# Kernel optimization log

Measured on AMD Instinct MI355X. Metric: run time of the kernel, lower is better.

## Reference

```python
import jax, jax.numpy as jnp
import numpy as np

M, IN, OUT = 8192, 4096, 4096
XOR_MASK = (1 << 3) | (1 << 7)  # 0x88: flips sign bit of each packed nibble


def _dequant_int4(weight_packed, weight_scales):
    """Decode packed int4 weights (offset-binary nibbles) to scaled float.

    weight_packed: [OUT, IN//2] int32, each byte holds two nibbles (v+8).
    Low nibble -> even input column, high nibble -> odd input column.
    """
    w = jnp.bitwise_xor(weight_packed, XOR_MASK)  # offset-binary -> two's complement nibbles
    low = jnp.bitwise_and(w, 0xF)
    high = jnp.bitwise_and(jnp.right_shift(w, 4), 0xF)
    low = jnp.where(low >= 8, low - 16, low)    # signed int4 in [-8, 7]
    high = jnp.where(high >= 8, high - 16, high)
    # interleave nibbles: [OUT, IN//2, 2] -> [OUT, IN]
    deq = jnp.stack([low, high], axis=-1).reshape(weight_packed.shape[0], -1)
    return deq.astype(weight_scales.dtype) * weight_scales[:, None]  # [OUT, IN]


def setup_inputs() -> dict:
    key = jax.random.key(0)
    k1, k2, k3, k4 = jax.random.split(key, 4)
    x = jax.random.normal(k1, (M, IN), dtype=jnp.float32)
    weight_packed = jax.random.randint(k2, (OUT, IN // 2), 0, 256, dtype=jnp.int32)
    weight_scales = jax.random.uniform(k3, (OUT,), dtype=jnp.float32) * 0.02 + 1e-3
    bias = jax.random.normal(k4, (OUT,), dtype=jnp.float32)
    return {"x": x, "weight_packed": weight_packed,
            "weight_scales": weight_scales, "bias": bias}


def reference(x, weight_packed, weight_scales, bias):
    # w4a16 forward: dequantize int4 weights per output row, then GEMM + bias.
    w = _dequant_int4(weight_packed, weight_scales)  # [OUT, IN]
    return jnp.dot(x, w.T) + bias  # [M, OUT]
```

## Files before the change

kernel.cpp:

```cpp
#include <hip/hip_runtime.h>
#include <cstdint>
#include <cstddef>

#define M_DIM 8192
#define K_DIM 4096
#define N_DIM 4096

#define BM 256
#define BN 256
#define BK 64
#define NT (K_DIM / BK)

typedef unsigned short u16;
typedef __bf16 bf16x8 __attribute__((ext_vector_type(8)));
typedef u16 u16x8 __attribute__((ext_vector_type(8)));
typedef float f32x4 __attribute__((ext_vector_type(4)));

__device__ __forceinline__ u16 f2bf_rne(float f) {
  uint32_t u = __builtin_bit_cast(uint32_t, f);
  return (u16)((u + 0x7FFFu + ((u >> 16) & 1u)) >> 16);
}
__device__ __forceinline__ u16 i2bf(int i) {
  return (u16)(__builtin_bit_cast(uint32_t, (float)i) >> 16);
}

#define XBLKS 16384
#define WBLKS 8192

__global__ __launch_bounds__(256) void prep(const float* __restrict__ x,
                                            const int* __restrict__ wp,
                                            u16* __restrict__ xb,
                                            u16* __restrict__ wb) {
  const int b = blockIdx.x;
  if (b < XBLKS) {
    size_t t = (size_t)b * 256 + threadIdx.x;
    const float4* xp = (const float4*)x;
    float4 a = xp[2 * t];
    float4 c = xp[2 * t + 1];
    u16x8 r;
    r[0] = f2bf_rne(a.x); r[1] = f2bf_rne(a.y); r[2] = f2bf_rne(a.z); r[3] = f2bf_rne(a.w);
    r[4] = f2bf_rne(c.x); r[5] = f2bf_rne(c.y); r[6] = f2bf_rne(c.z); r[7] = f2bf_rne(c.w);
    ((u16x8*)xb)[t] = r;
  } else {
    size_t t = (size_t)(b - XBLKS) * 256 + threadIdx.x;
    int4 p = ((const int4*)wp)[t];
    u16x8 r;
    int v;
    v = p.x ^ 0x88; r[0] = i2bf((v << 28) >> 28); r[1] = i2bf((v << 24) >> 28);
    v = p.y ^ 0x88; r[2] = i2bf((v << 28) >> 28); r[3] = i2bf((v << 24) >> 28);
    v = p.z ^ 0x88; r[4] = i2bf((v << 28) >> 28); r[5] = i2bf((v << 24) >> 28);
    v = p.w ^ 0x88; r[6] = i2bf((v << 28) >> 28); r[7] = i2bf((v << 24) >> 28);
    ((u16x8*)wb)[t] = r;
  }
}

__global__ __launch_bounds__(512, 2) void gemm_bt_w4a16(
    const u16* __restrict__ A,
    const u16* __restrict__ B,
    const float* __restrict__ scales,
    const float* __restrict__ bias,
    float* __restrict__ C) {
  __shared__ u16 sA0[3][128 * 64];
  __shared__ u16 sA1[2][128 * 64];
  __shared__ u16 sB0[2][128 * 64];
  __shared__ u16 sB1[2][128 * 64];

  const int tid = threadIdx.x;
  const int lane = tid & 63;
  const int wave = tid >> 6;
  const int m0 = blockIdx.y * BM;
  const int n0 = blockIdx.x * BN;

  const int wm = (wave >> 2) * 128;
  const int wn = (wave & 3) * 64;
  const int lrow = lane & 15;
  const int quad = lane >> 4;
  const int brw0 = wn & 64;

  f32x4 acc[8][4] = {};

  const int srow = tid >> 3;
  const int schunk = ((tid & 7) ^ (srow & 7)) * 8;
  const u16* ga = A + (size_t)(m0 + srow) * K_DIM + schunk;
  const u16* gb = B + (size_t)(n0 + srow) * K_DIM + schunk;
  const int dst0 = tid * 16;

#define GLDS(gp, lp)                                                      \
  __builtin_amdgcn_global_load_lds(                                       \
      (const __attribute__((address_space(1))) void*)(gp),                \
      (__attribute__((address_space(3))) void*)(lp), 16, 0, 0)

  auto stA0 = [&](int slot, int T) {
    const u16* g = ga + (size_t)T * BK;
    char* d = (char*)sA0[slot] + dst0;
    GLDS(g, d);
    GLDS(g + (size_t)64 * K_DIM, d + 8192);
  };
  auto stA1 = [&](int b, int T) {
    const u16* g = ga + (size_t)128 * K_DIM + (size_t)T * BK;
    char* d = (char*)sA1[b] + dst0;
    GLDS(g, d);
    GLDS(g + (size_t)64 * K_DIM, d + 8192);
  };
  auto stB0 = [&](int b, int T) {
    const u16* g = gb + (size_t)T * BK;
    char* d = (char*)sB0[b] + dst0;
    GLDS(g, d);
    GLDS(g + (size_t)64 * K_DIM, d + 8192);
  };
  auto stB1 = [&](int b, int T) {
    const u16* g = gb + (size_t)128 * K_DIM + (size_t)T * BK;
    char* d = (char*)sB1[b] + dst0;
    GLDS(g, d);
    GLDS(g + (size_t)64 * K_DIM, d + 8192);
  };

  struct frag4 { u16x8 v[4]; };

  stA0(0, 0); stA1(0, 0); stB0(0, 0); stB1(0, 0);

  int a0slot = 0;
#pragma unroll 1
  for (int T = 0; T < NT; ++T) {
    const int buf = T & 1;
    const int nbuf = buf ^ 1;
    const bool more = (T + 1 < NT);
    int a0next = a0slot + 1; if (a0next == 3) a0next = 0;

    if (more) {
      stA0(a0next, T + 1);
      asm volatile("s_waitcnt vmcnt(2)" ::: "memory");
    } else {
      asm volatile("s_waitcnt vmcnt(0)" ::: "memory");
    }
    __builtin_amdgcn_s_barrier();
    __builtin_amdgcn_sched_barrier(0);

    const u16* aH = (wave < 4) ? sA0[a0slot] : sA1[buf];
    const u16* bH = (wn < 128) ? sB0[buf] : sB1[buf];

    const int kc0 = ((0 * 4 + quad) ^ (lrow & 7)) * 8;
    const int kc1 = ((1 * 4 + quad) ^ (lrow & 7)) * 8;

    auto ldA = [&](int ih, int kc) {
      frag4 f;
#pragma unroll
      for (int i = 0; i < 4; ++i)
        f.v[i] = *(const u16x8*)(aH + (ih * 64 + i * 16 + lrow) * BK + kc);
      return f;
    };
    auto ldB = [&](int kc) {
      frag4 f;
#pragma unroll
      for (int j = 0; j < 4; ++j)
        f.v[j] = *(const u16x8*)(bH + (brw0 + j * 16 + lrow) * BK + kc);
      return f;
    };

    frag4 bfr0 = ldB(kc0);
    frag4 afA = ldA(0, kc0);

    frag4 afB = ldA(1, kc0);
    if (more) stA1(nbuf, T + 1);
    __builtin_amdgcn_s_setprio(1);
#pragma unroll
    for (int i = 0; i < 4; ++i)
#pragma unroll
      for (int j = 0; j < 4; ++j)
        acc[i][j] = __builtin_amdgcn_mfma_f32_16x16x32_bf16(
            __builtin_bit_cast(bf16x8, afA.v[i]),
            __builtin_bit_cast(bf16x8, bfr0.v[j]), acc[i][j], 0, 0, 0);
    __builtin_amdgcn_s_setprio(0);

    frag4 afA2 = ldA(0, kc1);
    frag4 bfr1 = ldB(kc1);
    if (more) stB0(nbuf, T + 1);
    __builtin_amdgcn_s_setprio(1);
#pragma unroll
    for (int i = 0; i < 4; ++i)
#pragma unroll
      for (int j = 0; j < 4; ++j)
        acc[4 + i][j] = __builtin_amdgcn_mfma_f32_16x16x32_bf16(
            __builtin_bit_cast(bf16x8, afB.v[i]),
            __builtin_bit_cast(bf16x8, bfr0.v[j]), acc[4 + i][j], 0, 0, 0);
    __builtin_amdgcn_s_setprio(0);

    frag4 afB2 = ldA(1, kc1);
    if (more) stB1(nbuf, T + 1);
    __builtin_amdgcn_s_setprio(1);
#pragma unroll
    for (int i = 0; i < 4; ++i)
#pragma unroll
      for (int j = 0; j < 4; ++j)
        acc[i][j] = __builtin_amdgcn_mfma_f32_16x16x32_bf16(
            __builtin_bit_cast(bf16x8, afA2.v[i]),
            __builtin_bit_cast(bf16x8, bfr1.v[j]), acc[i][j], 0, 0, 0);
    __builtin_amdgcn_s_setprio(0);

    __builtin_amdgcn_s_setprio(1);
#pragma unroll
    for (int i = 0; i < 4; ++i)
#pragma unroll
      for (int j = 0; j < 4; ++j)
        acc[4 + i][j] = __builtin_amdgcn_mfma_f32_16x16x32_bf16(
            __builtin_bit_cast(bf16x8, afB2.v[i]),
            __builtin_bit_cast(bf16x8, bfr1.v[j]), acc[4 + i][j], 0, 0, 0);
    __builtin_amdgcn_s_setprio(0);

    __builtin_amdgcn_sched_barrier(0);
    a0slot = a0next;
  }

#pragma unroll
  for (int j = 0; j < 4; ++j) {
    const int n = n0 + wn + j * 16 + lrow;
    const float sc = scales[n];
    const float bi = bias[n];
#pragma unroll
    for (int i = 0; i < 8; ++i) {
      const int m = m0 + wm + i * 16 + quad * 4;
      float* cp = &C[(size_t)m * N_DIM + n];
#pragma unroll
      for (int r = 0; r < 4; ++r)
        cp[(size_t)r * N_DIM] = acc[i][j][r] * sc + bi;
    }
  }
#undef GLDS
}

__global__ __launch_bounds__(256) void fallback_w4a16(
    const float* __restrict__ x, const int* __restrict__ wp,
    const float* __restrict__ scales, const float* __restrict__ bias,
    float* __restrict__ out) {
  const int n = blockIdx.x * 256 + threadIdx.x;
  const int m = blockIdx.y;
  const float* xr = x + (size_t)m * K_DIM;
  const int* wr = wp + (size_t)n * (K_DIM / 2);
  float acc = 0.f;
  for (int j = 0; j < K_DIM / 2; ++j) {
    int w = wr[j] ^ 0x88;
    float lo = (float)((w << 28) >> 28);
    float hi = (float)((w << 24) >> 28);
    acc += xr[2 * j] * lo + xr[2 * j + 1] * hi;
  }
  out[(size_t)m * N_DIM + n] = acc * scales[n] + bias[n];
}

extern "C" void kernel_launch(void* const* d_in, const int* in_sizes, int n_in,
                              void* d_out, int out_size, void* d_ws, size_t ws_size,
                              hipStream_t stream) {
  const float* x = (const float*)d_in[0];
  const int* wp = (const int*)d_in[1];
  const float* sc = (const float*)d_in[2];
  const float* bi = (const float*)d_in[3];
  float* out = (float*)d_out;

  const size_t xb_elems = (size_t)M_DIM * K_DIM;
  const size_t wb_elems = (size_t)N_DIM * K_DIM;
  const size_t need = (xb_elems + wb_elems) * sizeof(u16);

  if (ws_size >= need) {
    u16* xb = (u16*)d_ws;
    u16* wb = xb + xb_elems;
    prep<<<XBLKS + WBLKS, 256, 0, stream>>>(x, wp, xb, wb);
    gemm_bt_w4a16<<<dim3(N_DIM / BN, M_DIM / BM), 512, 0, stream>>>(xb, wb, sc, bi, out);
  } else {
    fallback_w4a16<<<dim3(N_DIM / 256, M_DIM), 256, 0, stream>>>(x, wp, sc, bi, out);
  }
}
```

Before: 460.0 us.

## Fuse fp32-to-bf16 activation conversion into GEMM mainloop via register staging

Drops the separate x-to-bf16 prep pass, so the workspace no longer holds a converted copy of x. The GEMM now loads fp32 activation tiles into registers two iterations ahead, converts them with packed bf16 conversion instructions, and writes them to LDS inside the K loop. The weight tiles still use direct global-to-LDS loads, and the shared-memory buffers are restructured into plain double buffers. This removes a full write and re-read of a 64MB bf16 activation tensor, in exchange for more registers, VALU conversion work and LDS stores in the hot loop, plus twice the global read bytes for A per tile.

Result: slower. 513.0 us (+11.5%).

```diff
diff --git a/kernel.cpp b/kernel.cpp
--- a/kernel.cpp
+++ b/kernel.cpp
@@ -16,54 +16,38 @@
 typedef u16 u16x8 __attribute__((ext_vector_type(8)));
 typedef float f32x4 __attribute__((ext_vector_type(4)));
 
-__device__ __forceinline__ u16 f2bf_rne(float f) {
-  uint32_t u = __builtin_bit_cast(uint32_t, f);
-  return (u16)((u + 0x7FFFu + ((u >> 16) & 1u)) >> 16);
-}
 __device__ __forceinline__ u16 i2bf(int i) {
   return (u16)(__builtin_bit_cast(uint32_t, (float)i) >> 16);
 }
-
-#define XBLKS 16384
+__device__ __forceinline__ uint32_t cvt2(float a, float b) {
+  uint32_t r;
+  asm("v_cvt_pk_bf16_f32 %0, %1, %2" : "=v"(r) : "v"(a), "v"(b));
+  return r;
+}
+
 #define WBLKS 8192
 
-__global__ __launch_bounds__(256) void prep(const float* __restrict__ x,
-                                            const int* __restrict__ wp,
-                                            u16* __restrict__ xb,
+__global__ __launch_bounds__(256) void prep(const int* __restrict__ wp,
                                             u16* __restrict__ wb) {
-  const int b = blockIdx.x;
-  if (b < XBLKS) {
-    size_t t = (size_t)b * 256 + threadIdx.x;
-    const float4* xp = (const float4*)x;
-    float4 a = xp[2 * t];
-    float4 c = xp[2 * t + 1];
-    u16x8 r;
-    r[0] = f2bf_rne(a.x); r[1] = f2bf_rne(a.y); r[2] = f2bf_rne(a.z); r[3] = f2bf_rne(a.w);
-    r[4] = f2bf_rne(c.x); r[5] = f2bf_rne(c.y); r[6] = f2bf_rne(c.z); r[7] = f2bf_rne(c.w);
-    ((u16x8*)xb)[t] = r;
-  } else {
-    size_t t = (size_t)(b - XBLKS) * 256 + threadIdx.x;
-    int4 p = ((const int4*)wp)[t];
-    u16x8 r;
-    int v;
-    v = p.x ^ 0x88; r[0] = i2bf((v << 28) >> 28); r[1] = i2bf((v << 24) >> 28);
-    v = p.y ^ 0x88; r[2] = i2bf((v << 28) >> 28); r[3] = i2bf((v << 24) >> 28);
-    v = p.z ^ 0x88; r[4] = i2bf((v << 28) >> 28); r[5] = i2bf((v << 24) >> 28);
-    v = p.w ^ 0x88; r[6] = i2bf((v << 28) >> 28); r[7] = i2bf((v << 24) >> 28);
-    ((u16x8*)wb)[t] = r;
-  }
-}
-
-__global__ __launch_bounds__(512, 2) void gemm_bt_w4a16(
-    const u16* __restrict__ A,
+  size_t t = (size_t)blockIdx.x * 256 + threadIdx.x;
+  int4 p = ((const int4*)wp)[t];
+  u16x8 r;
+  int v;
+  v = p.x ^ 0x88; r[0] = i2bf((v << 28) >> 28); r[1] = i2bf((v << 24) >> 28);
+  v = p.y ^ 0x88; r[2] = i2bf((v << 28) >> 28); r[3] = i2bf((v << 24) >> 28);
+  v = p.z ^ 0x88; r[4] = i2bf((v << 28) >> 28); r[5] = i2bf((v << 24) >> 28);
+  v = p.w ^ 0x88; r[6] = i2bf((v << 28) >> 28); r[7] = i2bf((v << 24) >> 28);
+  ((u16x8*)wb)[t] = r;
+}
+
+__global__ __launch_bounds__(512, 2) void gemm_w4a16_fused(
+    const float* __restrict__ X,
     const u16* __restrict__ B,
     const float* __restrict__ scales,
     const float* __restrict__ bias,
     float* __restrict__ C) {
-  __shared__ u16 sA0[3][128 * 64];
-  __shared__ u16 sA1[2][128 * 64];
-  __shared__ u16 sB0[2][128 * 64];
-  __shared__ u16 sB1[2][128 * 64];
+  __shared__ u16 sA[2][2 * 8192];
+  __shared__ u16 sB[2][2 * 8192];
 
   const int tid = threadIdx.x;
   const int lane = tid & 63;
@@ -81,7 +65,7 @@
 
   const int srow = tid >> 3;
   const int schunk = ((tid & 7) ^ (srow & 7)) * 8;
-  const u16* ga = A + (size_t)(m0 + srow) * K_DIM + schunk;
+  const float* gx = X + (size_t)(m0 + srow) * K_DIM + schunk;
   const u16* gb = B + (size_t)(n0 + srow) * K_DIM + schunk;
   const int dst0 = tid * 16;
 
@@ -90,66 +74,89 @@
       (const __attribute__((address_space(1))) void*)(gp),                \
       (__attribute__((address_space(3))) void*)(lp), 16, 0, 0)
 
-  auto stA0 = [&](int slot, int T) {
-    const u16* g = ga + (size_t)T * BK;
-    char* d = (char*)sA0[slot] + dst0;
+  auto stB0 = [&](int nb, int T) {
+    const u16* g = gb + (size_t)T * BK;
+    char* d = (char*)sB[nb] + dst0;
     GLDS(g, d);
     GLDS(g + (size_t)64 * K_DIM, d + 8192);
   };
-  auto stA1 = [&](int b, int T) {
-    const u16* g = ga + (size_t)128 * K_DIM + (size_t)T * BK;
-    char* d = (char*)sA1[b] + dst0;
+  auto stB1 = [&](int nb, int T) {
+    const u16* g = gb + (size_t)128 * K_DIM + (size_t)T * BK;
+    char* d = (char*)sB[nb] + 16384 + dst0;
     GLDS(g, d);
     GLDS(g + (size_t)64 * K_DIM, d + 8192);
   };
-  auto stB0 = [&](int b, int T) {
-    const u16* g = gb + (size_t)T * BK;
-    char* d = (char*)sB0[b] + dst0;
-    GLDS(g, d);
-    GLDS(g + (size_t)64 * K_DIM, d + 8192);
-  };
-  auto stB1 = [&](int b, int T) {
-    const u16* g = gb + (size_t)128 * K_DIM + (size_t)T * BK;
-    char* d = (char*)sB1[b] + dst0;
-    GLDS(g, d);
-    GLDS(g + (size_t)64 * K_DIM, d + 8192);
+
+  struct C8 { float4 lo, hi; };
+  C8 c00, c01, c10, c11;
+  auto ldA = [&](int T) {
+    const float* p = gx + (size_t)T * BK;
+    c00.lo = *(const float4*)(p);
+    c00.hi = *(const float4*)(p + 4);
+    const float* p1 = p + (size_t)64 * K_DIM;
+    c01.lo = *(const float4*)(p1);
+    c01.hi = *(const float4*)(p1 + 4);
+    const float* p2 = p + (size_t)128 * K_DIM;
+    c10.lo = *(const float4*)(p2);
+    c10.hi = *(const float4*)(p2 + 4);
+    const float* p3 = p + (size_t)192 * K_DIM;
+    c11.lo = *(const float4*)(p3);
+    c11.hi = *(const float4*)(p3 + 4);
+  };
+  auto wrA = [&](int nb) {
+    uint4 q;
+    char* d = (char*)sA[nb] + dst0;
+    q.x = cvt2(c00.lo.x, c00.lo.y); q.y = cvt2(c00.lo.z, c00.lo.w);
+    q.z = cvt2(c00.hi.x, c00.hi.y); q.w = cvt2(c00.hi.z, c00.hi.w);
+    *(uint4*)(d) = q;
+    q.x = cvt2(c01.lo.x, c01.lo.y); q.y = cvt2(c01.lo.z, c01.lo.w);
+    q.z = cvt2(c01.hi.x, c01.hi.y); q.w = cvt2(c01.hi.z, c01.hi.w);
+    *(uint4*)(d + 8192) = q;
+    q.x = cvt2(c10.lo.x, c10.lo.y); q.y = cvt2(c10.lo.z, c10.lo.w);
+    q.z = cvt2(c10.hi.x, c10.hi.y); q.w = cvt2(c10.hi.z, c10.hi.w);
+    *(uint4*)(d + 16384) = q;
+    q.x = cvt2(c11.lo.x, c11.lo.y); q.y = cvt2(c11.lo.z, c11.lo.w);
+    q.z = cvt2(c11.hi.x, c11.hi.y); q.w = cvt2(c11.hi.z, c11.hi.w);
+    *(uint4*)(d + 24576) = q;
   };
 
   struct frag4 { u16x8 v[4]; };
 
-  stA0(0, 0); stA1(0, 0); stB0(0, 0); stB1(0, 0);
-
-  int a0slot = 0;
+  ldA(0);
+  stB0(0, 0); stB1(0, 0);
+  wrA(0);
+  __builtin_amdgcn_sched_barrier(0);
+  ldA(1);
+
 #pragma unroll 1
   for (int T = 0; T < NT; ++T) {
-    const int buf = T & 1;
-    const int nbuf = buf ^ 1;
+    const int cb = T & 1;
+    const int nb = cb ^ 1;
     const bool more = (T + 1 < NT);
-    int a0next = a0slot + 1; if (a0next == 3) a0next = 0;
-
-    if (more) {
-      stA0(a0next, T + 1);
-      asm volatile("s_waitcnt vmcnt(2)" ::: "memory");
-    } else {
-      asm volatile("s_waitcnt vmcnt(0)" ::: "memory");
-    }
+
+    if (more)
+      asm volatile("s_waitcnt vmcnt(8) lgkmcnt(0)" ::: "memory");
+    else
+      asm volatile("s_waitcnt vmcnt(0) lgkmcnt(0)" ::: "memory");
     __builtin_amdgcn_s_barrier();
     __builtin_amdgcn_sched_barrier(0);
 
-    const u16* aH = (wave < 4) ? sA0[a0slot] : sA1[buf];
-    const u16* bH = (wn < 128) ? sB0[buf] : sB1[buf];
+    if (more) stB0(nb, T + 1);
+
+    const u16* aH = sA[cb] + ((wave >> 2) ? 8192 : 0);
+    const u16* bH = sB[cb] + ((wn & 128) ? 8192 : 0);
 
     const int kc0 = ((0 * 4 + quad) ^ (lrow & 7)) * 8;
     const int kc1 = ((1 * 4 + quad) ^ (lrow & 7)) * 8;
 
-    auto ldA = [&](int ih, int kc) {
+    auto ldAf = [&](int ih, int kc) {
       frag4 f;
 #pragma unroll
       for (int i = 0; i < 4; ++i)
         f.v[i] = *(const u16x8*)(aH + (ih * 64 + i * 16 + lrow) * BK + kc);
       return f;
     };
-    auto ldB = [&](int kc) {
+    auto ldBf = [&](int kc) {
       frag4 f;
 #pragma unroll
       for (int j = 0; j < 4; ++j)
@@ -157,11 +164,10 @@
       return f;
     };
 
-    frag4 bfr0 = ldB(kc0);
-    frag4 afA = ldA(0, kc0);
-
-    frag4 afB = ldA(1, kc0);
-    if (more) stA1(nbuf, T + 1);
+    frag4 bfr0 = ldBf(kc0);
+    frag4 afA = ldAf(0, kc0);
+
+    frag4 afB = ldAf(1, kc0);
     __builtin_amdgcn_s_setprio(1);
 #pragma unroll
     for (int i = 0; i < 4; ++i)
@@ -172,9 +178,9 @@
             __builtin_bit_cast(bf16x8, bfr0.v[j]), acc[i][j], 0, 0, 0);
     __builtin_amdgcn_s_setprio(0);
 
-    frag4 afA2 = ldA(0, kc1);
-    frag4 bfr1 = ldB(kc1);
-    if (more) stB0(nbuf, T + 1);
+    frag4 afA2 = ldAf(0, kc1);
+    frag4 bfr1 = ldBf(kc1);
+    if (more) stB1(nb, T + 1);
     __builtin_amdgcn_s_setprio(1);
 #pragma unroll
     for (int i = 0; i < 4; ++i)
@@ -185,8 +191,8 @@
             __builtin_bit_cast(bf16x8, bfr0.v[j]), acc[4 + i][j], 0, 0, 0);
     __builtin_amdgcn_s_setprio(0);
 
-    frag4 afB2 = ldA(1, kc1);
-    if (more) stB1(nbuf, T + 1);
+    frag4 afB2 = ldAf(1, kc1);
+    if (more) wrA(nb);
     __builtin_amdgcn_s_setprio(1);
 #pragma unroll
     for (int i = 0; i < 4; ++i)
@@ -208,7 +214,8 @@
     __builtin_amdgcn_s_setprio(0);
 
     __builtin_amdgcn_sched_barrier(0);
-    a0slot = a0next;
+    if (T + 2 < NT) ldA(T + 2);
+    __builtin_amdgcn_sched_barrier(0);
   }
 
 #pragma unroll
@@ -255,15 +262,13 @@
   const float* bi = (const float*)d_in[3];
   float* out = (float*)d_out;
 
-  const size_t xb_elems = (size_t)M_DIM * K_DIM;
   const size_t wb_elems = (size_t)N_DIM * K_DIM;
-  const size_t need = (xb_elems + wb_elems) * sizeof(u16);
+  const size_t need = wb_elems * sizeof(u16);
 
   if (ws_size >= need) {
-    u16* xb = (u16*)d_ws;
-    u16* wb = xb + xb_elems;
-    prep<<<XBLKS + WBLKS, 256, 0, stream>>>(x, wp, xb, wb);
-    gemm_bt_w4a16<<<dim3(N_DIM / BN, M_DIM / BM), 512, 0, stream>>>(xb, wb, sc, bi, out);
+    u16* wb = (u16*)d_ws;
+    prep<<<WBLKS, 256, 0, stream>>>(wp, wb);
+    gemm_w4a16_fused<<<dim3(N_DIM / BN, M_DIM / BM), 512, 0, stream>>>(x, wb, sc, bi, out);
   } else {
     fallback_w4a16<<<dim3(N_DIM / 256, M_DIM), 256, 0, stream>>>(x, wp, sc, bi, out);
   }
```

## Use 4 waves with 128x128 warp tiles instead of 8 waves with 128x64

Applied to the files above, without the earlier changes.

Halves the workgroup to 256 threads and gives each wave a 128x128 output tile (8x8 MFMA accumulators) instead of 128x64. Each wave now reads 8 A and 8 B fragments per k-half, so LDS reads per MFMA drop. Each thread issues four global-to-LDS loads per stage instead of two, and the vmcnt wait is adjusted to match. The cost is a large accumulator footprint (256 VGPRs) with only 4 waves per block, which risks spills or too little latency hiding.

Result: slower. 1.114 ms (+142.1%).

```diff
diff --git a/kernel.cpp b/kernel.cpp
--- a/kernel.cpp
+++ b/kernel.cpp
@@ -54,7 +54,7 @@
   }
 }
 
-__global__ __launch_bounds__(512, 2) void gemm_bt_w4a16(
+__global__ __launch_bounds__(256, 1) void gemm_bt_w4a16(
     const u16* __restrict__ A,
     const u16* __restrict__ B,
     const float* __restrict__ scales,
@@ -71,13 +71,12 @@
   const int m0 = blockIdx.y * BM;
   const int n0 = blockIdx.x * BN;
 
-  const int wm = (wave >> 2) * 128;
-  const int wn = (wave & 3) * 64;
+  const int wm = (wave >> 1) * 128;
+  const int wn = (wave & 1) * 128;
   const int lrow = lane & 15;
   const int quad = lane >> 4;
-  const int brw0 = wn & 64;
-
-  f32x4 acc[8][4] = {};
+
+  f32x4 acc[8][8] = {};
 
   const int srow = tid >> 3;
   const int schunk = ((tid & 7) ^ (srow & 7)) * 8;
@@ -93,29 +92,29 @@
   auto stA0 = [&](int slot, int T) {
     const u16* g = ga + (size_t)T * BK;
     char* d = (char*)sA0[slot] + dst0;
-    GLDS(g, d);
-    GLDS(g + (size_t)64 * K_DIM, d + 8192);
+#pragma unroll
+    for (int r = 0; r < 4; ++r) GLDS(g + (size_t)(r * 32) * K_DIM, d + r * 4096);
   };
   auto stA1 = [&](int b, int T) {
     const u16* g = ga + (size_t)128 * K_DIM + (size_t)T * BK;
     char* d = (char*)sA1[b] + dst0;
-    GLDS(g, d);
-    GLDS(g + (size_t)64 * K_DIM, d + 8192);
+#pragma unroll
+    for (int r = 0; r < 4; ++r) GLDS(g + (size_t)(r * 32) * K_DIM, d + r * 4096);
   };
   auto stB0 = [&](int b, int T) {
     const u16* g = gb + (size_t)T * BK;
     char* d = (char*)sB0[b] + dst0;
-    GLDS(g, d);
-    GLDS(g + (size_t)64 * K_DIM, d + 8192);
+#pragma unroll
+    for (int r = 0; r < 4; ++r) GLDS(g + (size_t)(r * 32) * K_DIM, d + r * 4096);
   };
   auto stB1 = [&](int b, int T) {
     const u16* g = gb + (size_t)128 * K_DIM + (size_t)T * BK;
     char* d = (char*)sB1[b] + dst0;
-    GLDS(g, d);
-    GLDS(g + (size_t)64 * K_DIM, d + 8192);
-  };
-
-  struct frag4 { u16x8 v[4]; };
+#pragma unroll
+    for (int r = 0; r < 4; ++r) GLDS(g + (size_t)(r * 32) * K_DIM, d + r * 4096);
+  };
+
+  struct frag8 { u16x8 v[8]; };
 
   stA0(0, 0); stA1(0, 0); stB0(0, 0); stB1(0, 0);
 
@@ -129,82 +128,80 @@
 
     if (more) {
       stA0(a0next, T + 1);
-      asm volatile("s_waitcnt vmcnt(2)" ::: "memory");
+      asm volatile("s_waitcnt vmcnt(4)" ::: "memory");
     } else {
       asm volatile("s_waitcnt vmcnt(0)" ::: "memory");
     }
     __builtin_amdgcn_s_barrier();
     __builtin_amdgcn_sched_barrier(0);
 
-    const u16* aH = (wave < 4) ? sA0[a0slot] : sA1[buf];
-    const u16* bH = (wn < 128) ? sB0[buf] : sB1[buf];
+    const u16* aH = (wm == 0) ? sA0[a0slot] : sA1[buf];
+    const u16* bH = (wn == 0) ? sB0[buf] : sB1[buf];
 
     const int kc0 = ((0 * 4 + quad) ^ (lrow & 7)) * 8;
     const int kc1 = ((1 * 4 + quad) ^ (lrow & 7)) * 8;
 
-    auto ldA = [&](int ih, int kc) {
-      frag4 f;
-#pragma unroll
-      for (int i = 0; i < 4; ++i)
-        f.v[i] = *(const u16x8*)(aH + (ih * 64 + i * 16 + lrow) * BK + kc);
+    auto ldA8 = [&](int kc) {
+      frag8 f;
+#pragma unroll
+      for (int i = 0; i < 8; ++i)
+        f.v[i] = *(const u16x8*)(aH + (i * 16 + lrow) * BK + kc);
       return f;
     };
-    auto ldB = [&](int kc) {
-      frag4 f;
-#pragma unroll
-      for (int j = 0; j < 4; ++j)
-        f.v[j] = *(const u16x8*)(bH + (brw0 + j * 16 + lrow) * BK + kc);
+    auto ldB8 = [&](int kc) {
+      frag8 f;
+#pragma unroll
+      for (int j = 0; j < 8; ++j)
+        f.v[j] = *(const u16x8*)(bH + (j * 16 + lrow) * BK + kc);
       return f;
     };
 
-    frag4 bfr0 = ldB(kc0);
-    frag4 afA = ldA(0, kc0);
-
-    frag4 afB = ldA(1, kc0);
+    frag8 fa0 = ldA8(kc0);
+    frag8 fb0 = ldB8(kc0);
+
     if (more) stA1(nbuf, T + 1);
     __builtin_amdgcn_s_setprio(1);
 #pragma unroll
     for (int i = 0; i < 4; ++i)
 #pragma unroll
-      for (int j = 0; j < 4; ++j)
+      for (int j = 0; j < 8; ++j)
         acc[i][j] = __builtin_amdgcn_mfma_f32_16x16x32_bf16(
-            __builtin_bit_cast(bf16x8, afA.v[i]),
-            __builtin_bit_cast(bf16x8, bfr0.v[j]), acc[i][j], 0, 0, 0);
-    __builtin_amdgcn_s_setprio(0);
-
-    frag4 afA2 = ldA(0, kc1);
-    frag4 bfr1 = ldB(kc1);
+            __builtin_bit_cast(bf16x8, fa0.v[i]),
+            __builtin_bit_cast(bf16x8, fb0.v[j]), acc[i][j], 0, 0, 0);
+    __builtin_amdgcn_s_setprio(0);
+
+    frag8 fa1 = ldA8(kc1);
     if (more) stB0(nbuf, T + 1);
     __builtin_amdgcn_s_setprio(1);
 #pragma unroll
     for (int i = 0; i < 4; ++i)
 #pragma unroll
-      for (int j = 0; j < 4; ++j)
+      for (int j = 0; j < 8; ++j)
         acc[4 + i][j] = __builtin_amdgcn_mfma_f32_16x16x32_bf16(
-            __builtin_bit_cast(bf16x8, afB.v[i]),
-            __builtin_bit_cast(bf16x8, bfr0.v[j]), acc[4 + i][j], 0, 0, 0);
-    __builtin_amdgcn_s_setprio(0);
-
-    frag4 afB2 = ldA(1, kc1);
+            __builtin_bit_cast(bf16x8, fa0.v[4 + i]),
+            __builtin_bit_cast(bf16x8, fb0.v[j]), acc[4 + i][j], 0, 0, 0);
+    __builtin_amdgcn_s_setprio(0);
+
+    frag8 fb1 = ldB8(kc1);
     if (more) stB1(nbuf, T + 1);
     __builtin_amdgcn_s_setprio(1);
 #pragma unroll
     for (int i = 0; i < 4; ++i)
 #pragma unroll
-      for (int j = 0; j < 4; ++j)
+      for (int j = 0; j < 8; ++j)
         acc[i][j] = __builtin_amdgcn_mfma_f32_16x16x32_bf16(
-            __builtin_bit_cast(bf16x8, afA2.v[i]),
-            __builtin_bit_cast(bf16x8, bfr1.v[j]), acc[i][j], 0, 0, 0);
-    __builtin_amdgcn_s_setprio(0);
-
-    __builtin_amdgcn_s_setprio(1);
-#pragma unroll
-    for (int i = 0; i < 4; ++i)
-#pragma unroll
-      for (int j = 0; j < 4; ++j)
+            __builtin_bit_cast(bf16x8, fa1.v[i]),
+            __builtin_bit_cast(bf16x8, fb1.v[j]), acc[i][j], 0, 0, 0);
+    __builtin_amdgcn_s_setprio(0);
+
+    __builtin_amdgcn_s_setprio(1);
+#pragma unroll
+    for (int i = 0; i < 4; ++i)
+#pragma unroll
+      for (int j = 0; j < 8; ++j)
         acc[4 + i][j] = __builtin_amdgcn_mfma_f32_16x16x32_bf16(
-            __builtin_bit_cast(bf16x8, afB2.v[i]),
-            __builtin_bit_cast(bf16x8, bfr1.v[j]), acc[4 + i][j], 0, 0, 0);
+            __builtin_bit_cast(bf16x8, fa1.v[4 + i]),
+            __builtin_bit_cast(bf16x8, fb1.v[j]), acc[4 + i][j], 0, 0, 0);
     __builtin_amdgcn_s_setprio(0);
 
     __builtin_amdgcn_sched_barrier(0);
@@ -212,7 +209,7 @@
   }
 
 #pragma unroll
-  for (int j = 0; j < 4; ++j) {
+  for (int j = 0; j < 8; ++j) {
     const int n = n0 + wn + j * 16 + lrow;
     const float sc = scales[n];
     const float bi = bias[n];
@@ -263,7 +260,7 @@
     u16* xb = (u16*)d_ws;
     u16* wb = xb + xb_elems;
     prep<<<XBLKS + WBLKS, 256, 0, stream>>>(x, wp, xb, wb);
-    gemm_bt_w4a16<<<dim3(N_DIM / BN, M_DIM / BM), 512, 0, stream>>>(xb, wb, sc, bi, out);
+    gemm_bt_w4a16<<<dim3(N_DIM / BN, M_DIM / BM), 256, 0, stream>>>(xb, wb, sc, bi, out);
   } else {
     fallback_w4a16<<<dim3(N_DIM / 256, M_DIM), 256, 0, stream>>>(x, wp, sc, bi, out);
   }
```

## Restructure main loop into barrier-gated phases with explicit LDS waits

Applied to the files above, without the earlier changes.

Reorganizes each K-iteration into four phases. Each phase issues its LDS fragment reads and next-tile global-to-LDS loads, then passes a workgroup barrier plus an lgkmcnt(0) wait before running a 16-MFMA cluster, with another barrier after it. This is a ping-pong style schedule meant to keep waves in lockstep so that memory and compute phases interleave across the two co-resident blocks. The cost is several extra barriers per iteration, and waiting for all LDS reads before compute removes the previous overlap of loads with MFMAs inside a wave.

After: 497.0 us. +8.0%, slower.

```diff
diff --git a/kernel.cpp b/kernel.cpp
--- a/kernel.cpp
+++ b/kernel.cpp
@@ -117,6 +117,23 @@
 
   struct frag4 { u16x8 v[4]; };
 
+#define PHASE_GATE()                                       \
+  __builtin_amdgcn_s_barrier();                            \
+  asm volatile("s_waitcnt lgkmcnt(0)" ::: "memory");       \
+  __builtin_amdgcn_sched_barrier(0)
+
+#define CLUSTER16(fa, fb, base)                                           \
+  __builtin_amdgcn_s_setprio(1);                                          \
+  _Pragma("unroll")                                                       \
+  for (int i = 0; i < 4; ++i)                                             \
+    _Pragma("unroll")                                                     \
+    for (int j = 0; j < 4; ++j)                                           \
+      acc[(base) + i][j] = __builtin_amdgcn_mfma_f32_16x16x32_bf16(       \
+          __builtin_bit_cast(bf16x8, (fa).v[i]),                          \
+          __builtin_bit_cast(bf16x8, (fb).v[j]), acc[(base) + i][j],      \
+          0, 0, 0);                                                       \
+  __builtin_amdgcn_s_setprio(0)
+
   stA0(0, 0); stA1(0, 0); stB0(0, 0); stB1(0, 0);
 
   int a0slot = 0;
@@ -159,53 +176,27 @@
 
     frag4 bfr0 = ldB(kc0);
     frag4 afA = ldA(0, kc0);
+    if (more) stA1(nbuf, T + 1);
+    PHASE_GATE();
+    CLUSTER16(afA, bfr0, 0);
+    __builtin_amdgcn_s_barrier();
 
     frag4 afB = ldA(1, kc0);
-    if (more) stA1(nbuf, T + 1);
-    __builtin_amdgcn_s_setprio(1);
-#pragma unroll
-    for (int i = 0; i < 4; ++i)
-#pragma unroll
-      for (int j = 0; j < 4; ++j)
-        acc[i][j] = __builtin_amdgcn_mfma_f32_16x16x32_bf16(
-            __builtin_bit_cast(bf16x8, afA.v[i]),
-            __builtin_bit_cast(bf16x8, bfr0.v[j]), acc[i][j], 0, 0, 0);
-    __builtin_amdgcn_s_setprio(0);
+    if (more) stB0(nbuf, T + 1);
+    PHASE_GATE();
+    CLUSTER16(afB, bfr0, 4);
+    __builtin_amdgcn_s_barrier();
 
     frag4 afA2 = ldA(0, kc1);
     frag4 bfr1 = ldB(kc1);
-    if (more) stB0(nbuf, T + 1);
-    __builtin_amdgcn_s_setprio(1);
-#pragma unroll
-    for (int i = 0; i < 4; ++i)
-#pragma unroll
-      for (int j = 0; j < 4; ++j)
-        acc[4 + i][j] = __builtin_amdgcn_mfma_f32_16x16x32_bf16(
-            __builtin_bit_cast(bf16x8, afB.v[i]),
-            __builtin_bit_cast(bf16x8, bfr0.v[j]), acc[4 + i][j], 0, 0, 0);
-    __builtin_amdgcn_s_setprio(0);
+    if (more) stB1(nbuf, T + 1);
+    PHASE_GATE();
+    CLUSTER16(afA2, bfr1, 0);
+    __builtin_amdgcn_s_barrier();
 
     frag4 afB2 = ldA(1, kc1);
-    if (more) stB1(nbuf, T + 1);
-    __builtin_amdgcn_s_setprio(1);
-#pragma unroll
-    for (int i = 0; i < 4; ++i)
-#pragma unroll
-      for (int j = 0; j < 4; ++j)
-        acc[i][j] = __builtin_amdgcn_mfma_f32_16x16x32_bf16(
-            __builtin_bit_cast(bf16x8, afA2.v[i]),
-            __builtin_bit_cast(bf16x8, bfr1.v[j]), acc[i][j], 0, 0, 0);
-    __builtin_amdgcn_s_setprio(0);
-
-    __builtin_amdgcn_s_setprio(1);
-#pragma unroll
-    for (int i = 0; i < 4; ++i)
-#pragma unroll
-      for (int j = 0; j < 4; ++j)
-        acc[4 + i][j] = __builtin_amdgcn_mfma_f32_16x16x32_bf16(
-            __builtin_bit_cast(bf16x8, afB2.v[i]),
-            __builtin_bit_cast(bf16x8, bfr1.v[j]), acc[4 + i][j], 0, 0, 0);
-    __builtin_amdgcn_s_setprio(0);
+    PHASE_GATE();
+    CLUSTER16(afB2, bfr1, 4);
 
     __builtin_amdgcn_sched_barrier(0);
     a0slot = a0next;
@@ -226,6 +217,8 @@
     }
   }
 #undef GLDS
+#undef PHASE_GATE
+#undef CLUSTER16
 }
 
 __global__ __launch_bounds__(256) void fallback_w4a16(
```
